# Performance work log

Measured on AMD Instinct MI355X. Metric: run time of the kernel, lower is better.

Reference implementation:

```python
import jax, jax.numpy as jnp
import numpy as np

NUM_HEADS = 16
HEAD_DIM = 64
INNER = NUM_HEADS * HEAD_DIM  # 1024
QUERY_DIM = 1024
CONTEXT_DIM = 768
SCALE = HEAD_DIM ** -0.5


def setup_inputs() -> dict:
    key = jax.random.key(0)
    ks = jax.random.split(key, 6)
    B, NQ, NKV = 8, 1024, 2048
    query = jax.random.normal(ks[0], (B, NQ, QUERY_DIM), dtype=jnp.float32)
    context = jax.random.normal(ks[1], (B, NKV, CONTEXT_DIM), dtype=jnp.float32)
    # weights stored as [in, out] (transpose of torch Linear), math-equivalent
    w_q = jax.random.normal(ks[2], (QUERY_DIM, INNER), dtype=jnp.float32) * (QUERY_DIM ** -0.5)
    w_kv = jax.random.normal(ks[3], (CONTEXT_DIM, 2 * INNER), dtype=jnp.float32) * (CONTEXT_DIM ** -0.5)
    w_out = jax.random.normal(ks[4], (INNER, QUERY_DIM), dtype=jnp.float32) * (INNER ** -0.5)
    b_out = jax.random.normal(ks[5], (QUERY_DIM,), dtype=jnp.float32) * 0.01
    return {"query": query, "context": context, "w_q": w_q, "w_kv": w_kv,
            "w_out": w_out, "b_out": b_out}


def reference(query, context, w_q, w_kv, w_out, b_out):
    B, NQ, _ = query.shape
    NKV = context.shape[1]
    q = query @ w_q                              # [B, NQ, INNER]
    kv = context @ w_kv                          # [B, NKV, 2*INNER]
    k, v = jnp.split(kv, 2, axis=-1)
    # reshape to [B, H, N, D]
    q = q.reshape(B, NQ, NUM_HEADS, HEAD_DIM).transpose(0, 2, 1, 3)
    k = k.reshape(B, NKV, NUM_HEADS, HEAD_DIM).transpose(0, 2, 1, 3)
    v = v.reshape(B, NKV, NUM_HEADS, HEAD_DIM).transpose(0, 2, 1, 3)
    scores = jnp.einsum('bhqd,bhkd->bhqk', q, k) * SCALE
    attn = jax.nn.softmax(scores, axis=-1)
    out = jnp.einsum('bhqk,bhkd->bhqd', attn, v)  # [B, H, NQ, D]
    out = out.transpose(0, 2, 1, 3).reshape(B, NQ, INNER)
    return out @ w_out + b_out
```

## Files before the change

kernel.cpp:

```cpp
#include <hip/hip_runtime.h>
#include <stdint.h>

typedef __bf16 bf16_t;
typedef bf16_t bf16x8 __attribute__((ext_vector_type(8)));
typedef float f32x4 __attribute__((ext_vector_type(4)));

__device__ __forceinline__ unsigned short f2bf(float x) {
    unsigned u = __builtin_bit_cast(unsigned, x);
    u = (u + 0x7FFFu + ((u >> 16) & 1u)) >> 16;
    return (unsigned short)u;
}

__device__ __forceinline__ unsigned pk_bf16(float lo, float hi) {
    unsigned u0 = __builtin_bit_cast(unsigned, lo) + 0x8000u;
    unsigned u1 = __builtin_bit_cast(unsigned, hi) + 0x8000u;
    return __builtin_amdgcn_perm(u1, u0, 0x07060302u);
}

__device__ __forceinline__ void async_load16(const void* g, void* lds) {
    auto* gp = reinterpret_cast<const __attribute__((address_space(1))) uint32_t*>(
        reinterpret_cast<uintptr_t>(g));
    auto* lp = reinterpret_cast<__attribute__((address_space(3))) uint32_t*>(
        reinterpret_cast<uintptr_t>(lds));
    __builtin_amdgcn_global_load_lds(gp, lp, 16, 0, 0);
}

__global__ __launch_bounds__(256) void cast_f32_bf16(const float* __restrict__ src,
                                                     unsigned short* __restrict__ dst,
                                                     int n8) {
    int i = blockIdx.x * 256 + threadIdx.x;
    if (i >= n8) return;
    const float4* s4 = (const float4*)src;
    float4 a = s4[i * 2], b = s4[i * 2 + 1];
    uint4 o;
    o.x = (unsigned)f2bf(a.x) | ((unsigned)f2bf(a.y) << 16);
    o.y = (unsigned)f2bf(a.z) | ((unsigned)f2bf(a.w) << 16);
    o.z = (unsigned)f2bf(b.x) | ((unsigned)f2bf(b.y) << 16);
    o.w = (unsigned)f2bf(b.z) | ((unsigned)f2bf(b.w) << 16);
    ((uint4*)dst)[i] = o;
}

__global__ __launch_bounds__(256) void transcast(const float* __restrict__ src,
                                                 unsigned short* __restrict__ dst,
                                                 int K, int N, float scale) {
    __shared__ float tile[32][33];
    int x = threadIdx.x, y = threadIdx.y;
    int c0 = blockIdx.x * 32, r0 = blockIdx.y * 32;
    #pragma unroll
    for (int i = 0; i < 32; i += 8)
        tile[y + i][x] = src[(size_t)(r0 + y + i) * N + c0 + x];
    __syncthreads();
    #pragma unroll
    for (int i = 0; i < 32; i += 8)
        dst[(size_t)(c0 + y + i) * K + r0 + x] = f2bf(tile[x][y + i] * scale);
}

template <int EPI>
__global__ __launch_bounds__(256) void gemm_bt(const unsigned short* __restrict__ A,
                                               const unsigned short* __restrict__ Bt,
                                               void* __restrict__ Cout,
                                               const float* __restrict__ bias,
                                               unsigned short* __restrict__ Vt,
                                               int K, int N, int nkt) {
    __shared__ __align__(16) unsigned short lA[128 * 64];
    __shared__ __align__(16) unsigned short lB[128 * 64];
    const int tid = threadIdx.x;
    const int w = tid >> 6, l = tid & 63;
    const int wm = w >> 1, wn = w & 1;
    const int row0 = blockIdx.y * 128, col0 = blockIdx.x * 128;
    const int lrow = l & 15, lq = l >> 4;
    const int srow = l >> 3;
    const int scol = ((l & 7) ^ srow) * 8;

    f32x4 acc[4][4];
    #pragma unroll
    for (int i = 0; i < 4; ++i)
        #pragma unroll
        for (int j = 0; j < 4; ++j) acc[i][j] = (f32x4)0.f;

    for (int kt = 0; kt < nkt; ++kt) {
        const int k0 = kt * 64;
        __syncthreads();
        #pragma unroll
        for (int q = 0; q < 4; ++q) {
            int r = (w * 4 + q) * 8 + srow;
            async_load16(A + (size_t)(row0 + r) * K + k0 + scol,
                         (char*)lA + (w * 4 + q) * 1024);
            async_load16(Bt + (size_t)(col0 + r) * K + k0 + scol,
                         (char*)lB + (w * 4 + q) * 1024);
        }
        __syncthreads();
        #pragma unroll
        for (int kc = 0; kc < 2; ++kc) {
            const int pc = ((kc * 4 + lq) ^ (lrow & 7)) * 16;
            bf16x8 af[4], bfr[4];
            #pragma unroll
            for (int i = 0; i < 4; ++i)
                af[i] = *(const bf16x8*)((const char*)lA + (wm * 64 + i * 16 + lrow) * 128 + pc);
            #pragma unroll
            for (int j = 0; j < 4; ++j)
                bfr[j] = *(const bf16x8*)((const char*)lB + (wn * 64 + j * 16 + lrow) * 128 + pc);
            #pragma unroll
            for (int i = 0; i < 4; ++i)
                #pragma unroll
                for (int j = 0; j < 4; ++j)
                    acc[i][j] = __builtin_amdgcn_mfma_f32_16x16x32_bf16(af[i], bfr[j],
                                                                        acc[i][j], 0, 0, 0);
        }
    }
    #pragma unroll
    for (int i = 0; i < 4; ++i) {
        const int grow0 = row0 + wm * 64 + i * 16 + lq * 4;
        #pragma unroll
        for (int j = 0; j < 4; ++j) {
            const int gcol = col0 + wn * 64 + j * 16 + lrow;
            #pragma unroll
            for (int r = 0; r < 4; ++r) {
                float v = acc[i][j][r];
                int grow = grow0 + r;
                if (EPI == 0) {
                    ((unsigned short*)Cout)[(size_t)grow * N + gcol] = f2bf(v);
                } else if (EPI == 1) {
                    if (gcol < 1024) {
                        ((unsigned short*)Cout)[(size_t)grow * 1024 + gcol] = f2bf(v);
                    } else {
                        int b = grow >> 11, key = grow & 2047;
                        Vt[((size_t)(b * 1024 + (gcol - 1024))) * 2048 + key] = f2bf(v);
                    }
                } else {
                    ((float*)Cout)[(size_t)grow * N + gcol] = v + bias[gcol];
                }
            }
        }
    }
}

__global__ __launch_bounds__(256, 4) void attn_fwd(const unsigned short* __restrict__ qb,
                                                   const unsigned short* __restrict__ kb,
                                                   const unsigned short* __restrict__ vt,
                                                   unsigned short* __restrict__ ob) {
    constexpr int PSTR = 72;
    __shared__ __align__(16) unsigned short lK[64 * 64];
    __shared__ __align__(16) unsigned short lV[64 * 64];
    __shared__ __align__(16) unsigned short lP[4][32 * PSTR];
    const int tid = threadIdx.x;
    const int w = tid >> 6, l = tid & 63;
    const int b = blockIdx.z, h = blockIdx.y, q0 = blockIdx.x * 128;
    const int lrow = l & 15, lq = l >> 4;
    const int srow = l >> 3, scol = ((l & 7) ^ (srow & 7)) * 8;

    bf16x8 bq[2][2];
    #pragma unroll
    for (int qs = 0; qs < 2; ++qs)
        #pragma unroll
        for (int kc = 0; kc < 2; ++kc) {
            int row = b * 1024 + q0 + w * 32 + qs * 16 + lrow;
            int col = h * 64 + kc * 32 + lq * 8;
            bq[qs][kc] = *(const bf16x8*)(qb + (size_t)row * 1024 + col);
        }

    f32x4 ot[2][4];
    f32x4 lsv[2];
    #pragma unroll
    for (int qs = 0; qs < 2; ++qs) {
        #pragma unroll
        for (int dt = 0; dt < 4; ++dt) ot[qs][dt] = (f32x4)0.f;
        lsv[qs] = (f32x4)0.f;
    }

    const char* kp0 = (const char*)lK + lrow * 128 + ((lq ^ (lrow & 7)) * 16);
    const char* kp1 = (const char*)lK + lrow * 128 + (((4 + lq) ^ (lrow & 7)) * 16);
    const char* vp0 = (const char*)lV + lrow * 128 + ((lq ^ (lrow & 7)) * 16);
    const char* vp1 = (const char*)lV + lrow * 128 + (((4 + lq) ^ (lrow & 7)) * 16);
    char* pw[2];
    const char* pr[2];
    #pragma unroll
    for (int qs = 0; qs < 2; ++qs) {
        pw[qs] = (char*)&lP[w][(qs * 16 + lrow) * PSTR + 4 * lq];
        pr[qs] = (const char*)&lP[w][(qs * 16 + lrow) * PSTR + 8 * lq];
    }

    const unsigned short* gkp = kb + (size_t)b * 2048 * 1024 + h * 64 +
                                (size_t)(w * 8 + srow) * 1024 + scol;
    const unsigned short* gvp = vt + (size_t)(b * 1024 + h * 64) * 2048 +
                                (size_t)(w * 8 + srow) * 2048 + scol;
    char* lKw0 = (char*)lK + (w * 8) * 128;
    char* lKw1 = (char*)lK + (32 + w * 8) * 128;
    char* lVw0 = (char*)lV + (w * 8) * 128;
    char* lVw1 = (char*)lV + (32 + w * 8) * 128;

    for (int it = 0; it < 32; ++it) {
        __syncthreads();
        async_load16(gkp, lKw0);
        async_load16(gkp + 32 * 1024, lKw1);
        async_load16(gvp, lVw0);
        async_load16(gvp + 32 * 2048, lVw1);
        gkp += 64 * 1024;
        gvp += 64;
        __syncthreads();

        f32x4 st[2][4];
        #pragma unroll
        for (int mt = 0; mt < 4; ++mt) {
            bf16x8 ka0 = *(const bf16x8*)(kp0 + mt * 2048);
            bf16x8 ka1 = *(const bf16x8*)(kp1 + mt * 2048);
            #pragma unroll
            for (int qs = 0; qs < 2; ++qs) {
                f32x4 c = (f32x4)0.f;
                c = __builtin_amdgcn_mfma_f32_16x16x32_bf16(ka0, bq[qs][0], c, 0, 0, 0);
                c = __builtin_amdgcn_mfma_f32_16x16x32_bf16(ka1, bq[qs][1], c, 0, 0, 0);
                st[qs][mt] = c;
            }
        }

        #pragma unroll
        for (int qs = 0; qs < 2; ++qs) {
            #pragma unroll
            for (int mt = 0; mt < 4; ++mt)
                #pragma unroll
                for (int r = 0; r < 4; ++r)
                    st[qs][mt][r] = __builtin_amdgcn_exp2f(st[qs][mt][r]);
            lsv[qs] += (st[qs][0] + st[qs][1]) + (st[qs][2] + st[qs][3]);
            #pragma unroll
            for (int mt = 0; mt < 4; ++mt) {
                uint2 pk;
                pk.x = pk_bf16(st[qs][mt][0], st[qs][mt][1]);
                pk.y = pk_bf16(st[qs][mt][2], st[qs][mt][3]);
                *(uint2*)(pw[qs] + 32 * mt) = pk;
            }
        }

        bf16x8 pb[2][2];
        #pragma unroll
        for (int qs = 0; qs < 2; ++qs)
            #pragma unroll
            for (int kcg = 0; kcg < 2; ++kcg)
                pb[qs][kcg] = *(const bf16x8*)(pr[qs] + 64 * kcg);

        #pragma unroll
        for (int dt = 0; dt < 4; ++dt) {
            bf16x8 va0 = *(const bf16x8*)(vp0 + dt * 2048);
            bf16x8 va1 = *(const bf16x8*)(vp1 + dt * 2048);
            #pragma unroll
            for (int qs = 0; qs < 2; ++qs) {
                ot[qs][dt] = __builtin_amdgcn_mfma_f32_16x16x32_bf16(va0, pb[qs][0], ot[qs][dt], 0, 0, 0);
                ot[qs][dt] = __builtin_amdgcn_mfma_f32_16x16x32_bf16(va1, pb[qs][1], ot[qs][dt], 0, 0, 0);
            }
        }
    }

    #pragma unroll
    for (int qs = 0; qs < 2; ++qs) {
        float rs = (lsv[qs][0] + lsv[qs][1]) + (lsv[qs][2] + lsv[qs][3]);
        rs += __shfl_xor(rs, 16);
        rs += __shfl_xor(rs, 32);
        float inv = 1.f / rs;
        size_t grow = (size_t)(b * 1024 + q0 + w * 32 + qs * 16 + lrow);
        unsigned short* op = ob + grow * 1024 + h * 64 + 4 * lq;
        #pragma unroll
        for (int dt = 0; dt < 4; ++dt) {
            uint2 pk;
            pk.x = pk_bf16(ot[qs][dt][0] * inv, ot[qs][dt][1] * inv);
            pk.y = pk_bf16(ot[qs][dt][2] * inv, ot[qs][dt][3] * inv);
            *(uint2*)(op + 16 * dt) = pk;
        }
    }
}

extern "C" void kernel_launch(void* const* d_in, const int* in_sizes, int n_in,
                              void* d_out, int out_size, void* d_ws, size_t ws_size,
                              hipStream_t stream) {
    const float* query   = (const float*)d_in[0];
    const float* context = (const float*)d_in[1];
    const float* w_q     = (const float*)d_in[2];
    const float* w_kv    = (const float*)d_in[3];
    const float* w_out   = (const float*)d_in[4];
    const float* b_out   = (const float*)d_in[5];
    float* out = (float*)d_out;

    char* p = (char*)d_ws;
    unsigned short* qin   = (unsigned short*)p; p += (size_t)8192 * 1024 * 2;
    unsigned short* cin   = (unsigned short*)p; p += (size_t)16384 * 768 * 2;
    unsigned short* wqT   = (unsigned short*)p; p += (size_t)1024 * 1024 * 2;
    unsigned short* wkvT  = (unsigned short*)p; p += (size_t)2048 * 768 * 2;
    unsigned short* woutT = (unsigned short*)p; p += (size_t)1024 * 1024 * 2;
    unsigned short* qproj = (unsigned short*)p; p += (size_t)8192 * 1024 * 2;
    unsigned short* kbuf  = (unsigned short*)p; p += (size_t)16384 * 1024 * 2;
    unsigned short* vT    = (unsigned short*)p; p += (size_t)16384 * 1024 * 2;
    unsigned short* obuf  = (unsigned short*)p; p += (size_t)8192 * 1024 * 2;

    const float qscale = 0.125f * 1.44269504088896f;

    cast_f32_bf16<<<8388608 / 8 / 256, 256, 0, stream>>>(query, qin, 8388608 / 8);
    cast_f32_bf16<<<12582912 / 8 / 256, 256, 0, stream>>>(context, cin, 12582912 / 8);
    transcast<<<dim3(32, 32), dim3(32, 8), 0, stream>>>(w_q, wqT, 1024, 1024, qscale);
    transcast<<<dim3(64, 24), dim3(32, 8), 0, stream>>>(w_kv, wkvT, 768, 2048, 1.0f);
    transcast<<<dim3(32, 32), dim3(32, 8), 0, stream>>>(w_out, woutT, 1024, 1024, 1.0f);
    gemm_bt<0><<<dim3(8, 64), 256, 0, stream>>>(qin, wqT, qproj, nullptr, nullptr, 1024, 1024, 16);
    gemm_bt<1><<<dim3(16, 128), 256, 0, stream>>>(cin, wkvT, kbuf, nullptr, vT, 768, 2048, 12);
    attn_fwd<<<dim3(8, 16, 8), 256, 0, stream>>>(qproj, kbuf, vT, obuf);
    gemm_bt<2><<<dim3(8, 64), 256, 0, stream>>>(obuf, woutT, out, b_out, nullptr, 1024, 1024, 16);
}
```

Before: 391.7 us.

## Add dedicated KV projection GEMM with 32x32 MFMA and vectorized V-transpose stores

Replaces the generic EPI==1 path of gemm_bt with a specialized gemm_kv kernel. It uses 256x128 block tiles, 32x32x16 bf16 MFMA instructions and 4x2 accumulator tiles per wave. The V-transpose epilogue now packs four consecutive keys into 8-byte stores instead of scattered 2-byte writes, cutting uncoalesced global traffic. The larger tiles raise register and LDS use, so launch bounds drop to 2 blocks per CU, which may reduce occupancy.

```diff
diff --git a/kernel.cpp b/kernel.cpp
--- a/kernel.cpp
+++ b/kernel.cpp
@@ -4,6 +4,7 @@
 typedef __bf16 bf16_t;
 typedef bf16_t bf16x8 __attribute__((ext_vector_type(8)));
 typedef float f32x4 __attribute__((ext_vector_type(4)));
+typedef float f32x16 __attribute__((ext_vector_type(16)));
 
 __device__ __forceinline__ unsigned short f2bf(float x) {
     unsigned u = __builtin_bit_cast(unsigned, x);
@@ -60,7 +61,6 @@
                                                const unsigned short* __restrict__ Bt,
                                                void* __restrict__ Cout,
                                                const float* __restrict__ bias,
-                                               unsigned short* __restrict__ Vt,
                                                int K, int N, int nkt) {
     __shared__ __align__(16) unsigned short lA[128 * 64];
     __shared__ __align__(16) unsigned short lB[128 * 64];
@@ -120,18 +120,98 @@
                 int grow = grow0 + r;
                 if (EPI == 0) {
                     ((unsigned short*)Cout)[(size_t)grow * N + gcol] = f2bf(v);
-                } else if (EPI == 1) {
-                    if (gcol < 1024) {
-                        ((unsigned short*)Cout)[(size_t)grow * 1024 + gcol] = f2bf(v);
-                    } else {
-                        int b = grow >> 11, key = grow & 2047;
-                        Vt[((size_t)(b * 1024 + (gcol - 1024))) * 2048 + key] = f2bf(v);
-                    }
                 } else {
                     ((float*)Cout)[(size_t)grow * N + gcol] = v + bias[gcol];
                 }
             }
         }
+    }
+}
+
+__global__ __launch_bounds__(256, 2) void gemm_kv(const unsigned short* __restrict__ A,
+                                                  const unsigned short* __restrict__ Bt,
+                                                  unsigned short* __restrict__ Kb,
+                                                  unsigned short* __restrict__ Vt) {
+    __shared__ __align__(16) unsigned short lA[256 * 64];
+    __shared__ __align__(16) unsigned short lB[128 * 64];
+    const int tid = threadIdx.x;
+    const int w = tid >> 6, l = tid & 63;
+    const int wm = w >> 1, wn = w & 1;
+    const int row0 = blockIdx.y * 256, col0 = blockIdx.x * 128;
+    const int r32 = l & 31, hw = l >> 5;
+    const int srow = l >> 3, scol = ((l & 7) ^ srow) * 8;
+
+    f32x16 acc[4][2];
+    #pragma unroll
+    for (int mi = 0; mi < 4; ++mi)
+        #pragma unroll
+        for (int ni = 0; ni < 2; ++ni) acc[mi][ni] = (f32x16)0.f;
+
+    const unsigned short* ga = A + (size_t)(row0 + w * 8 + srow) * 768 + scol;
+    const unsigned short* gb = Bt + (size_t)(col0 + w * 8 + srow) * 768 + scol;
+    char* lAw = (char*)lA + (w * 8) * 128;
+    char* lBw = (char*)lB + (w * 8) * 128;
+    const char* lap = (const char*)lA + (wm * 128 + r32) * 128;
+    const char* lbp = (const char*)lB + (wn * 64 + r32) * 128;
+    const int r7 = r32 & 7;
+
+    for (int kt = 0; kt < 12; ++kt) {
+        __syncthreads();
+        #pragma unroll
+        for (int q = 0; q < 8; ++q)
+            async_load16(ga + (size_t)q * 32 * 768, lAw + q * 32 * 128);
+        #pragma unroll
+        for (int q = 0; q < 4; ++q)
+            async_load16(gb + (size_t)q * 32 * 768, lBw + q * 32 * 128);
+        ga += 64;
+        gb += 64;
+        __syncthreads();
+        #pragma unroll
+        for (int ks = 0; ks < 4; ++ks) {
+            const int off = ((ks * 2 + hw) ^ r7) * 16;
+            bf16x8 af[4], bfr[2];
+            #pragma unroll
+            for (int mi = 0; mi < 4; ++mi)
+                af[mi] = *(const bf16x8*)(lap + mi * 32 * 128 + off);
+            #pragma unroll
+            for (int ni = 0; ni < 2; ++ni)
+                bfr[ni] = *(const bf16x8*)(lbp + ni * 32 * 128 + off);
+            #pragma unroll
+            for (int mi = 0; mi < 4; ++mi)
+                #pragma unroll
+                for (int ni = 0; ni < 2; ++ni)
+                    acc[mi][ni] = __builtin_amdgcn_mfma_f32_32x32x16_bf16(af[mi], bfr[ni],
+                                                                          acc[mi][ni], 0, 0, 0);
+        }
+    }
+
+    if (col0 < 1024) {
+        unsigned short* kp = Kb + (size_t)(row0 + wm * 128) * 1024 + col0 + wn * 64 + r32;
+        #pragma unroll
+        for (int mi = 0; mi < 4; ++mi)
+            #pragma unroll
+            for (int ni = 0; ni < 2; ++ni)
+                #pragma unroll
+                for (int reg = 0; reg < 16; ++reg) {
+                    int rr = mi * 32 + (reg & 3) + 8 * (reg >> 2) + 4 * hw;
+                    kp[(size_t)rr * 1024 + ni * 32] = f2bf(acc[mi][ni][reg]);
+                }
+    } else {
+        const int bb = row0 >> 11;
+        const int keybase = (row0 & 2047) + wm * 128 + 4 * hw;
+        const int fvbase = col0 - 1024 + wn * 64 + r32;
+        unsigned short* vp = Vt + ((size_t)bb * 1024 + fvbase) * 2048 + keybase;
+        #pragma unroll
+        for (int mi = 0; mi < 4; ++mi)
+            #pragma unroll
+            for (int ni = 0; ni < 2; ++ni)
+                #pragma unroll
+                for (int g = 0; g < 4; ++g) {
+                    uint2 pk2;
+                    pk2.x = pk_bf16(acc[mi][ni][g * 4 + 0], acc[mi][ni][g * 4 + 1]);
+                    pk2.y = pk_bf16(acc[mi][ni][g * 4 + 2], acc[mi][ni][g * 4 + 3]);
+                    *(uint2*)(vp + (size_t)(ni * 32) * 2048 + mi * 32 + g * 8) = pk2;
+                }
     }
 }
 
@@ -296,8 +376,8 @@
     transcast<<<dim3(32, 32), dim3(32, 8), 0, stream>>>(w_q, wqT, 1024, 1024, qscale);
     transcast<<<dim3(64, 24), dim3(32, 8), 0, stream>>>(w_kv, wkvT, 768, 2048, 1.0f);
     transcast<<<dim3(32, 32), dim3(32, 8), 0, stream>>>(w_out, woutT, 1024, 1024, 1.0f);
-    gemm_bt<0><<<dim3(8, 64), 256, 0, stream>>>(qin, wqT, qproj, nullptr, nullptr, 1024, 1024, 16);
-    gemm_bt<1><<<dim3(16, 128), 256, 0, stream>>>(cin, wkvT, kbuf, nullptr, vT, 768, 2048, 12);
+    gemm_bt<0><<<dim3(8, 64), 256, 0, stream>>>(qin, wqT, qproj, nullptr, 1024, 1024, 16);
+    gemm_kv<<<dim3(16, 64), 256, 0, stream>>>(cin, wkvT, kbuf, vT);
     attn_fwd<<<dim3(8, 16, 8), 256, 0, stream>>>(qproj, kbuf, vT, obuf);
-    gemm_bt<2><<<dim3(8, 64), 256, 0, stream>>>(obuf, woutT, out, b_out, nullptr, 1024, 1024, 16);
-}
+    gemm_bt<2><<<dim3(8, 64), 256, 0, stream>>>(obuf, woutT, out, b_out, 1024, 1024, 16);
+}
```

After: 364.2 us. 1.08x faster.
